# Performance work log

Hardware: AMD Instinct MI355X
Metric: run time of the kernel (lower is better)

## Reference

```python
import jax, jax.numpy as jnp
import numpy as np

B, N, T, F = 4, 5000, 16, 64
E = 80000
H, C_OUT = 4, 16           # attention heads, per-head out channels
S = H * C_OUT              # stream_dim = 64
HID = 192                  # encoder hidden_dim = 3 * S
NEG_SLOPE = 0.2
EPS_SM = 1e-16             # PyG softmax eps
EPS_LN = 1e-5


def setup_inputs() -> dict:
    key = jax.random.key(0)
    ks = jax.random.split(key, 12)
    rn = lambda k, shape, s=0.1: jax.random.normal(k, shape, jnp.float32) * s
    return {
        "x_seq": rn(ks[0], (T, B, N, F), 1.0),
        "lin_w": rn(ks[1], (3, S, F)),          # per-stream GAT linear [out,in]
        "att_src": rn(ks[2], (3, H, C_OUT)),
        "att_dst": rn(ks[3], (3, H, C_OUT)),
        "gat_bias": jnp.zeros((3, S), jnp.float32),
        "w_ih": rn(ks[4], (3, 4 * S, S)),       # LSTMCell input weights (i,f,g,o)
        "w_hh": rn(ks[5], (3, 4 * S, S)),
        "b_ih": jnp.zeros((3, 4 * S), jnp.float32),
        "b_hh": jnp.zeros((3, 4 * S), jnp.float32),
        "ln_g": jnp.ones((3, S), jnp.float32),
        "ln_b": jnp.zeros((3, S), jnp.float32),
        "attn_w1": rn(ks[6], (HID // 2, 3 * S)),
        "attn_b1": jnp.zeros((HID // 2,), jnp.float32),
        "attn_w2": rn(ks[7], (3, HID // 2)),
        "attn_b2": jnp.zeros((3,), jnp.float32),
        "edge_index": jax.random.randint(ks[8], (2, E), 0, N, jnp.int32),
    }


def _batched_edges(edge_index):
    # replicate the graph B times with node-id offsets, then add self loops
    offs = (jnp.arange(B, dtype=edge_index.dtype) * N)[:, None]
    src = (edge_index[0][None, :] + offs).reshape(-1)
    dst = (edge_index[1][None, :] + offs).reshape(-1)
    loops = jnp.arange(B * N, dtype=edge_index.dtype)
    return jnp.concatenate([src, loops]), jnp.concatenate([dst, loops])


def _gat(x, src, dst, lin_w, a_src, a_dst, bias):
    # x: [B,N,F] -> out: [B,N,S]
    xt = (x.reshape(B * N, F) @ lin_w.T).reshape(B * N, H, C_OUT)
    xj, xi = xt[src], xt[dst]                               # [Eb,H,C]
    a = jnp.einsum('ehc,hc->eh', xj, a_src) + jnp.einsum('ehc,hc->eh', xi, a_dst)
    a = jax.nn.leaky_relu(a, NEG_SLOPE)
    amax = jax.ops.segment_max(a, dst, num_segments=B * N)  # segment-softmax over target
    ex = jnp.exp(a - amax[dst])
    den = jax.ops.segment_sum(ex, dst, num_segments=B * N)
    alpha = ex / (den[dst] + EPS_SM)
    out = jax.ops.segment_sum(xj * alpha[..., None], dst, num_segments=B * N)
    return out.reshape(B, N, S) + bias


def _cell(x, h, c, src, dst, lin_w, a_s, a_d, gb, wih, whh, bih, bhh, g, b):
    # one TemporalGNNCell step; h,c: [B*N,S]
    sp = _gat(x, src, dst, lin_w, a_s, a_d, gb).reshape(B * N, S)
    gates = sp @ wih.T + bih + h @ whh.T + bhh
    i, f, gg, o = jnp.split(gates, 4, axis=-1)
    c_new = jax.nn.sigmoid(f) * c + jax.nn.sigmoid(i) * jnp.tanh(gg)
    h_new = jax.nn.sigmoid(o) * jnp.tanh(c_new)
    mu = h_new.mean(-1, keepdims=True)
    var = ((h_new - mu) ** 2).mean(-1, keepdims=True)
    h_ln = (h_new - mu) / jnp.sqrt(var + EPS_LN) * g + b
    return h_ln, c_new


def reference(x_seq, lin_w, att_src, att_dst, gat_bias, w_ih, w_hh, b_ih, b_hh,
              ln_g, ln_b, attn_w1, attn_b1, attn_w2, attn_b2, edge_index):
    src, dst = _batched_edges(edge_index)
    z = jnp.zeros((B * N, S), x_seq.dtype)
    hf = cf = hm = cm = hs = cs = z
    outs = []
    for t in range(T):
        x_t = x_seq[t]
        hf, cf = _cell(x_t, hf, cf, src, dst, lin_w[0], att_src[0], att_dst[0], gat_bias[0],
                       w_ih[0], w_hh[0], b_ih[0], b_hh[0], ln_g[0], ln_b[0])
        if t % 15 == 0:
            hm, cm = _cell(x_t, hm, cm, src, dst, lin_w[1], att_src[1], att_dst[1], gat_bias[1],
                           w_ih[1], w_hh[1], b_ih[1], b_hh[1], ln_g[1], ln_b[1])
        if t % 150 == 0:
            hs, cs = _cell(x_t, hs, cs, src, dst, lin_w[2], att_src[2], att_dst[2], gat_bias[2],
                           w_ih[2], w_hh[2], b_ih[2], b_hh[2], ln_g[2], ln_b[2])
        fast, med, slow = hf, hm, hs
        ms = jnp.concatenate([fast, med, slow], axis=-1)       # [B*N, 3S]
        w = jax.nn.softmax(jax.nn.relu(ms @ attn_w1.T + attn_b1) @ attn_w2.T + attn_b2, axis=-1)
        outs.append(w[:, 0:1] * fast + w[:, 1:2] * med + w[:, 2:3] * slow)
    # stack(dim=1) then permute(0,2,1,3): [B, N, T, S]
    out = jnp.stack(outs, 0).reshape(T, B, N, S).transpose(1, 2, 0, 3)
    return out
```

## Files before the change

kernel.cpp:

```cpp
#include <hip/hip_runtime.h>
#include <cstddef>

#define TT 16
#define EE 80000
#define NB 768
#define HALF_N 2500
#define NCHUNK 157
#define NTILE 313
#define XT_PAR 320512
#define AS_PAR 20032
#define WBLK 258048
#define O_LINH 0
#define O_LINL 12288
#define O_WIHH 24576
#define O_WIHL 73728
#define O_WHHH 122880
#define O_WHHL 172032
#define O_W1H  221184
#define O_W1L  239616
#define XCCREG 6164

typedef __attribute__((ext_vector_type(8))) short bf16x8;
typedef __attribute__((ext_vector_type(4))) float f32x4;

__device__ __forceinline__ float sigf(float x) { return 1.0f / (1.0f + __expf(-x)); }
__device__ __forceinline__ float lreluf(float x) { return x > 0.0f ? x : 0.2f * x; }

__device__ __forceinline__ unsigned short f2bf(float x) {
  union { float f; unsigned u; } v; v.f = x;
  unsigned r = v.u + 0x7FFF + ((v.u >> 16) & 1);
  return (unsigned short)(r >> 16);
}
__device__ __forceinline__ float bf2f(unsigned short u) {
  union { unsigned u; float f; } v; v.u = ((unsigned)u) << 16; return v.f;
}
__device__ __forceinline__ unsigned short f2h(float x) {
  _Float16 h = (_Float16)x;
  return __builtin_bit_cast(unsigned short, h);
}
__device__ __forceinline__ float h2f(unsigned short u) {
  return (float)__builtin_bit_cast(_Float16, u);
}
__device__ __forceinline__ f32x4 mfma16(bf16x8 a, bf16x8 b, f32x4 c) {
  return __builtin_amdgcn_mfma_f32_16x16x32_bf16(a, b, c, 0, 0, 0);
}
__device__ __forceinline__ void split8(const float* s, bf16x8& th, bf16x8& tl) {
#pragma unroll
  for (int i = 0; i < 8; ++i) {
    float v = s[i];
    unsigned short h = f2bf(v);
    th[i] = (short)h;
    tl[i] = (short)f2bf(v - bf2f(h));
  }
}
__device__ __forceinline__ unsigned long long ldq(const void* p) {
  return __hip_atomic_load((unsigned long long*)p, __ATOMIC_RELAXED, __HIP_MEMORY_SCOPE_AGENT);
}
__device__ __forceinline__ float ldf(const float* p) {
  return __hip_atomic_load((float*)p, __ATOMIC_RELAXED, __HIP_MEMORY_SCOPE_AGENT);
}
__device__ __forceinline__ int ldi(const int* p) {
  return __hip_atomic_load((int*)p, __ATOMIC_RELAXED, __HIP_MEMORY_SCOPE_AGENT);
}
__device__ __forceinline__ float4 ldv4(const float* p) {
  union { unsigned long long q[2]; float4 v; } u;
  u.q[0] = ldq(p); u.q[1] = ldq(p + 2); return u.v;
}

struct P {
  const float *x_seq, *att_src, *att_dst, *gat_bias, *ln_g, *ln_b, *b1, *w2, *b2;
  const float *lin_w, *w_ih, *w_hh, *b_ih, *b_hh, *w1;
  const int* eidx;
  float* out;
  unsigned short* xt;
  float *as, *ad;
  float *cmg, *csg;
  unsigned short* wblk;
  float* bsum;
  int *deg, *cnt, *startp, *adj;
  int *reg, *gcnt, *ggen, *g0;
};

__device__ __forceinline__ void mbar(int* cnt, int* gen, int size, int& rnd) {
  __syncthreads();
  ++rnd;
  if (threadIdx.x == 0) {
    int v = __hip_atomic_fetch_add(cnt, 1, __ATOMIC_RELAXED, __HIP_MEMORY_SCOPE_AGENT) + 1;
    if (v == size * rnd) {
      __hip_atomic_store(gen, rnd, __ATOMIC_RELAXED, __HIP_MEMORY_SCOPE_AGENT);
    } else {
      while (__hip_atomic_load(gen, __ATOMIC_RELAXED, __HIP_MEMORY_SCOPE_AGENT) < rnd)
        __builtin_amdgcn_s_sleep(4);
    }
  }
  __builtin_amdgcn_fence(__ATOMIC_ACQUIRE, "workgroup");
  __syncthreads();
}

__device__ void phaseA(const float* xbase, const unsigned short* linH, const unsigned short* linL,
                       const float* attS, const float* attD,
                       unsigned short* xtC, float* asC, float* adC, int rb, int lane) {
  const int l15 = lane & 15, lg = lane >> 4;
  int gm = rb * 16 + l15; if (gm > 4999) gm = 4999;
  const float* arow = xbase + (size_t)gm * 64;
  bf16x8 aH[2], aL[2];
#pragma unroll
  for (int ch = 0; ch < 2; ++ch) {
    float4 u0 = *reinterpret_cast<const float4*>(arow + ch * 32 + lg * 8);
    float4 u1 = *reinterpret_cast<const float4*>(arow + ch * 32 + lg * 8 + 4);
    float v[8] = {u0.x, u0.y, u0.z, u0.w, u1.x, u1.y, u1.z, u1.w};
    bf16x8 th, tl;
#pragma unroll
    for (int i = 0; i < 8; ++i) {
      unsigned short hi = f2bf(v[i]);
      th[i] = (short)hi;
      tl[i] = (short)f2bf(v[i] - bf2f(hi));
    }
    aH[ch] = th; aL[ch] = tl;
  }
  f32x4 acc[4];
#pragma unroll
  for (int nf = 0; nf < 4; ++nf) acc[nf] = (f32x4){0.f, 0.f, 0.f, 0.f};
#pragma unroll
  for (int nf = 0; nf < 4; ++nf) {
#pragma unroll
    for (int ch = 0; ch < 2; ++ch) {
      size_t wo = (size_t)(nf * 16 + l15) * 64 + ch * 32 + lg * 8;
      bf16x8 bH = *reinterpret_cast<const bf16x8*>(linH + wo);
      bf16x8 bL = *reinterpret_cast<const bf16x8*>(linL + wo);
      acc[nf] = mfma16(aH[ch], bH, acc[nf]);
      acc[nf] = mfma16(aH[ch], bL, acc[nf]);
      acc[nf] = mfma16(aL[ch], bH, acc[nf]);
    }
  }
#pragma unroll
  for (int nf = 0; nf < 4; ++nf) {
    float sv = attS[nf * 16 + l15], dv = attD[nf * 16 + l15];
#pragma unroll
    for (int r = 0; r < 4; ++r) {
      int row = rb * 16 + lg * 4 + r;
      float v = acc[nf][r];
      float ps = v * sv, pd = v * dv;
#pragma unroll
      for (int off = 1; off < 16; off <<= 1) { ps += __shfl_xor(ps, off); pd += __shfl_xor(pd, off); }
      xtC[(size_t)row * 64 + nf * 16 + l15] = f2h(v);
      if (l15 == 0) { asC[row * 4 + nf] = ps; adC[row * 4 + nf] = pd; }
    }
  }
}

__device__ void gather_node(const int* startp, const int* adj,
                            const float* asr, const float* adt, const unsigned short* xtC,
                            const float* gbias, int nh, int half, int lane,
                            float* sprow, float* alds, int* slds) {
  int s0 = startp[nh];
  int dg = startp[nh + 1] - s0;
  int nloc = half * 2500 + nh;
  float4 adv = ldv4(adt + (size_t)nloc * 4);

  float ex0 = 0.f, ex1 = 0.f, ex2 = 0.f, ex3 = 0.f;
  int src0 = 0;
  if (lane < dg) {
    src0 = adj[s0 + lane];
    float4 av = ldv4(asr + (size_t)src0 * 4);
    ex0 = __expf(lreluf(av.x + adv.x));
    ex1 = __expf(lreluf(av.y + adv.y));
    ex2 = __expf(lreluf(av.z + adv.z));
    ex3 = __expf(lreluf(av.w + adv.w));
  }
  float dn0 = ex0, dn1 = ex1, dn2 = ex2, dn3 = ex3;
  for (int e = 64 + lane; e < dg; e += 64) {
    int src = adj[s0 + e];
    float4 av = ldv4(asr + (size_t)src * 4);
    dn0 += __expf(lreluf(av.x + adv.x));
    dn1 += __expf(lreluf(av.y + adv.y));
    dn2 += __expf(lreluf(av.z + adv.z));
    dn3 += __expf(lreluf(av.w + adv.w));
  }
#pragma unroll
  for (int off = 1; off < 64; off <<= 1) {
    dn0 += __shfl_xor(dn0, off);
    dn1 += __shfl_xor(dn1, off);
    dn2 += __shfl_xor(dn2, off);
    dn3 += __shfl_xor(dn3, off);
  }
  float rd0 = 1.0f / (dn0 + 1e-16f), rd1 = 1.0f / (dn1 + 1e-16f);
  float rd2 = 1.0f / (dn2 + 1e-16f), rd3 = 1.0f / (dn3 + 1e-16f);
  if (lane < dg) {
    *reinterpret_cast<float4*>(alds + lane * 4) =
        make_float4(ex0 * rd0, ex1 * rd1, ex2 * rd2, ex3 * rd3);
    slds[lane] = src0;
  }
  const int g = lane >> 4, c = lane & 15, head = c >> 2;
  float a0 = 0.f, a1 = 0.f, a2 = 0.f, a3 = 0.f;
  int dglim = dg < 64 ? dg : 64;
  for (int e = g; e < dglim; e += 4) {
    float alpha = alds[e * 4 + head];
    int src = slds[e];
    unsigned long long q = ldq(xtC + (size_t)src * 64 + c * 4);
    a0 = fmaf(alpha, h2f((unsigned short)(q)), a0);
    a1 = fmaf(alpha, h2f((unsigned short)(q >> 16)), a1);
    a2 = fmaf(alpha, h2f((unsigned short)(q >> 32)), a2);
    a3 = fmaf(alpha, h2f((unsigned short)(q >> 48)), a3);
  }
  if (dg > 64) {
    float rdh = head == 0 ? rd0 : head == 1 ? rd1 : head == 2 ? rd2 : rd3;
    float adh = head == 0 ? adv.x : head == 1 ? adv.y : head == 2 ? adv.z : adv.w;
    for (int e = 64 + g; e < dg; e += 4) {
      int src = adj[s0 + e];
      float av = ldf(asr + (size_t)src * 4 + head);
      float alpha = __expf(lreluf(av + adh)) * rdh;
      unsigned long long q = ldq(xtC + (size_t)src * 64 + c * 4);
      a0 = fmaf(alpha, h2f((unsigned short)(q)), a0);
      a1 = fmaf(alpha, h2f((unsigned short)(q >> 16)), a1);
      a2 = fmaf(alpha, h2f((unsigned short)(q >> 32)), a2);
      a3 = fmaf(alpha, h2f((unsigned short)(q >> 48)), a3);
    }
  }
  a0 += __shfl_xor(a0, 16); a0 += __shfl_xor(a0, 32);
  a1 += __shfl_xor(a1, 16); a1 += __shfl_xor(a1, 32);
  a2 += __shfl_xor(a2, 16); a2 += __shfl_xor(a2, 32);
  a3 += __shfl_xor(a3, 16); a3 += __shfl_xor(a3, 32);
  if (g == 0) {
    float4 bz = *reinterpret_cast<const float4*>(gbias + c * 4);
    *reinterpret_cast<float4*>(sprow + c * 4) =
        make_float4(a0 + bz.x, a1 + bz.y, a2 + bz.z, a3 + bz.w);
  }
}

__device__ void mixcore(const unsigned short* w1H, const unsigned short* w1L,
                        const float* b1, const float* w2, const float* b2, float* out,
                        size_t grow0, int validrows, int t, int lane,
                        const float* hf, const float* hm, const float* hs) {
  const int l15 = lane & 15, lg = lane >> 4;
  bf16x8 aH[3][2], aL[3][2];
#pragma unroll
  for (int ch = 0; ch < 2; ++ch) {
    split8(hf + l15 * 68 + ch * 32 + lg * 8, aH[0][ch], aL[0][ch]);
    split8(hm + l15 * 68 + ch * 32 + lg * 8, aH[1][ch], aL[1][ch]);
    split8(hs + l15 * 68 + ch * 32 + lg * 8, aH[2][ch], aL[2][ch]);
  }
  f32x4 acc[6];
#pragma unroll
  for (int nf = 0; nf < 6; ++nf) acc[nf] = (f32x4){0.f, 0.f, 0.f, 0.f};
#pragma unroll
  for (int nf = 0; nf < 6; ++nf) {
#pragma unroll
    for (int s = 0; s < 3; ++s) {
#pragma unroll
      for (int ch = 0; ch < 2; ++ch) {
        size_t wo = (size_t)(nf * 16 + l15) * 192 + s * 64 + ch * 32 + lg * 8;
        bf16x8 bH = *reinterpret_cast<const bf16x8*>(w1H + wo);
        bf16x8 bL = *reinterpret_cast<const bf16x8*>(w1L + wo);
        acc[nf] = mfma16(aH[s][ch], bH, acc[nf]);
        acc[nf] = mfma16(aH[s][ch], bL, acc[nf]);
        acc[nf] = mfma16(aL[s][ch], bH, acc[nf]);
      }
    }
  }
#pragma unroll
  for (int r = 0; r < 4; ++r) {
    float p0 = 0.f, p1 = 0.f, p2 = 0.f;
#pragma unroll
    for (int nf = 0; nf < 6; ++nf) {
      int n = nf * 16 + l15;
      float hdv = fmaxf(acc[nf][r] + b1[n], 0.f);
      p0 = fmaf(hdv, w2[n], p0);
      p1 = fmaf(hdv, w2[96 + n], p1);
      p2 = fmaf(hdv, w2[192 + n], p2);
    }
#pragma unroll
    for (int off = 1; off < 16; off <<= 1) {
      p0 += __shfl_xor(p0, off); p1 += __shfl_xor(p1, off); p2 += __shfl_xor(p2, off);
    }
    float q0 = p0 + b2[0], q1 = p1 + b2[1], q2 = p2 + b2[2];
    float mx = fmaxf(q0, fmaxf(q1, q2));
    float e0 = __expf(q0 - mx), e1 = __expf(q1 - mx), e2 = __expf(q2 - mx);
    float rs = 1.0f / (e0 + e1 + e2);
    float w0 = e0 * rs, w1v = e1 * rs, w2v = e2 * rs;
    int r16 = lg * 4 + r;
    if (r16 < validrows) {
      size_t ob = ((grow0 + r16) * TT + t) * 64;
#pragma unroll
      for (int q = 0; q < 4; ++q) {
        int col = l15 + 16 * q;
        float vf = hf[r16 * 68 + col];
        float vm = hm[r16 * 68 + col];
        float vs = hs[r16 * 68 + col];
        out[ob + col] = w0 * vf + w1v * vm + w2v * vs;
      }
    }
  }
}

__device__ void phaseC(const unsigned short* WihH, const unsigned short* WihL,
                       const unsigned short* WhhH, const unsigned short* WhhL,
                       const float* bsum, const float* lng, const float* lnb,
                       float* cglob, float creg[4][4],
                       size_t grow0, int validrows, int lane,
                       const float* sp, float* h) {
  const int l15 = lane & 15, lg = lane >> 4;
  bf16x8 sH[2], sL[2], hHa[2], hLa[2];
#pragma unroll
  for (int ch = 0; ch < 2; ++ch) {
    split8(sp + l15 * 68 + ch * 32 + lg * 8, sH[ch], sL[ch]);
    split8(h + l15 * 68 + ch * 32 + lg * 8, hHa[ch], hLa[ch]);
  }
  f32x4 acc[16];
#pragma unroll
  for (int nf = 0; nf < 16; ++nf) acc[nf] = (f32x4){0.f, 0.f, 0.f, 0.f};
#pragma unroll
  for (int nf = 0; nf < 16; ++nf) {
#pragma unroll
    for (int ch = 0; ch < 2; ++ch) {
      size_t wo = (size_t)(nf * 16 + l15) * 64 + ch * 32 + lg * 8;
      bf16x8 bH = *reinterpret_cast<const bf16x8*>(WihH + wo);
      bf16x8 bL = *reinterpret_cast<const bf16x8*>(WihL + wo);
      acc[nf] = mfma16(sH[ch], bH, acc[nf]);
      acc[nf] = mfma16(sH[ch], bL, acc[nf]);
      acc[nf] = mfma16(sL[ch], bH, acc[nf]);
      bf16x8 cH = *reinterpret_cast<const bf16x8*>(WhhH + wo);
      bf16x8 cL = *reinterpret_cast<const bf16x8*>(WhhL + wo);
      acc[nf] = mfma16(hHa[ch], cH, acc[nf]);
      acc[nf] = mfma16(hHa[ch], cL, acc[nf]);
      acc[nf] = mfma16(hLa[ch], cH, acc[nf]);
    }
  }
  float hn[4][4];
#pragma unroll
  for (int cq = 0; cq < 4; ++cq) {
    int col = cq * 16 + l15;
    float bi = bsum[col], bff = bsum[64 + col], bg = bsum[128 + col], bo = bsum[192 + col];
#pragma unroll
    for (int r = 0; r < 4; ++r) {
      int r16 = lg * 4 + r;
      float gi = acc[cq][r] + bi;
      float gf = acc[cq + 4][r] + bff;
      float gg = acc[cq + 8][r] + bg;
      float go = acc[cq + 12][r] + bo;
      float cold;
      if (cglob) {
        int crow = r16 < validrows ? r16 : validrows - 1;
        cold = ldf(cglob + (grow0 + crow) * 64 + col);
      } else cold = creg[cq][r];
      float cv = sigf(gf) * cold + sigf(gi) * tanhf(gg);
      if (cglob) { if (r16 < validrows) cglob[(grow0 + r16) * 64 + col] = cv; }
      else creg[cq][r] = cv;
      hn[cq][r] = sigf(go) * tanhf(cv);
    }
  }
#pragma unroll
  for (int r = 0; r < 4; ++r) {
    float s = hn[0][r] + hn[1][r] + hn[2][r] + hn[3][r];
#pragma unroll
    for (int off = 1; off < 16; off <<= 1) s += __shfl_xor(s, off);
    float mu = s * (1.0f / 64.0f);
    float vv = 0.f;
#pragma unroll
    for (int cq = 0; cq < 4; ++cq) { float d = hn[cq][r] - mu; vv += d * d; }
#pragma unroll
    for (int off = 1; off < 16; off <<= 1) vv += __shfl_xor(vv, off);
    float rstd = rsqrtf(vv * (1.0f / 64.0f) + 1e-5f);
#pragma unroll
    for (int cq = 0; cq < 4; ++cq) {
      int col = cq * 16 + l15;
      h[(lg * 4 + r) * 68 + col] = (hn[cq][r] - mu) * rstd * lng[col] + lnb[col];
    }
  }
}

__global__ __launch_bounds__(256, 3) void mega(P p) {
  const int tid = threadIdx.x, lane = tid & 63, wv = tid >> 6, pair = wv >> 1;
  __shared__ float s8[8][16][68];
  __shared__ float al[4][256];
  __shared__ int sr[4][64];
  __shared__ int shr[2];

  const int xcd = (int)(__builtin_amdgcn_s_getreg(XCCREG) & 7);
  if (tid == 0)
    shr[0] = (int)__hip_atomic_fetch_add(&p.reg[xcd], 1, __ATOMIC_RELAXED, __HIP_MEMORY_SCOPE_AGENT);

  int grnd = 0;
  mbar(p.g0, p.g0 + 16, NB, grnd);
  if (tid == 0) shr[1] = ldi(&p.reg[xcd]);
  __syncthreads();
  const int rank = shr[0], size = shr[1];
  const int batch = xcd >> 1, half = xcd & 1;
  const size_t nodeg = (size_t)batch * 5000 + (size_t)half * 2500;

  unsigned short* xtX = p.xt + (size_t)xcd * 6 * XT_PAR;
  float* asX = p.as + (size_t)xcd * 6 * AS_PAR;
  float* adX = p.ad + (size_t)xcd * 6 * AS_PAR;
  unsigned short* w = p.wblk + (size_t)xcd * WBLK;
  float* bsum = p.bsum + xcd * 768;
  int* deg = p.deg + xcd * 2504;
  int* cnt = p.cnt + xcd * 2504;
  int* startp = p.startp + xcd * 2504;
  int* adj = p.adj + (size_t)xcd * 82504;
  int* xc = p.gcnt + xcd * 16;
  int* xg = p.ggen + xcd * 16;
  int xrnd = 0;

  for (int i = tid; i < 8 * 16 * 68; i += 256) ((float*)s8)[i] = 0.f;
  float creg[4][4];
#pragma unroll
  for (int a = 0; a < 4; ++a)
#pragma unroll
    for (int r = 0; r < 4; ++r) creg[a][r] = 0.f;

  const int st = rank * 256 + tid, stride = size * 256;

  for (int i = st; i < 160000; i += stride) {
    p.cmg[nodeg * 64 + i] = 0.f;
    p.csg[nodeg * 64 + i] = 0.f;
  }
  for (int i = st; i < 2504; i += stride) { deg[i] = 0; cnt[i] = 0; }
  for (int i = st; i < 49152; i += stride) {
    if (i < 12288) { float v = p.lin_w[i]; unsigned short h = f2bf(v); w[O_LINH + i] = h; w[O_LINL + i] = f2bf(v - bf2f(h)); }
    { float v = p.w_ih[i]; unsigned short h = f2bf(v); w[O_WIHH + i] = h; w[O_WIHL + i] = f2bf(v - bf2f(h)); }
    { float v = p.w_hh[i]; unsigned short h = f2bf(v); w[O_WHHH + i] = h; w[O_WHHL + i] = f2bf(v - bf2f(h)); }
    if (i < 18432) { float v = p.w1[i]; unsigned short h = f2bf(v); w[O_W1H + i] = h; w[O_W1L + i] = f2bf(v - bf2f(h)); }
    if (i < 768) bsum[i] = p.b_ih[i] + p.b_hh[i];
  }
  mbar(xc, xg, size, xrnd);

  for (int i = st; i < EE + 2500; i += stride) {
    if (i < EE) {
      int dst = p.eidx[EE + i];
      if ((dst >= 2500) == (half == 1)) atomicAdd(deg + (dst - half * 2500), 1);
    } else atomicAdd(deg + (i - EE), 1);
  }
  mbar(xc, xg, size, xrnd);

  if (rank == 0) {
    int* ib = (int*)&al[0][0];
    int s = 0;
    for (int j = 0; j < 10; ++j) {
      int n = tid * 10 + j;
      if (n < 2500) s += ldi(deg + n);
    }
    ib[tid] = s;
    __syncthreads();
    for (int off = 1; off < 256; off <<= 1) {
      int tv = (tid >= off) ? ib[tid - off] : 0;
      __syncthreads();
      ib[tid] += tv;
      __syncthreads();
    }
    int excl = ib[tid] - s;
    for (int j = 0; j < 10; ++j) {
      int n = tid * 10 + j;
      if (n < 2500) { startp[n] = excl; excl += ldi(deg + n); }
    }
    if (tid == 255) startp[2500] = ib[255];
    __syncthreads();
  }
  mbar(xc, xg, size, xrnd);

  for (int i = st; i < EE + 2500; i += stride) {
    if (i < EE) {
      int dst = p.eidx[EE + i];
      if ((dst >= 2500) == (half == 1)) {
        int ln = dst - half * 2500;
        int pos = atomicAdd(cnt + ln, 1);
        adj[startp[ln] + pos] = p.eidx[i];
      }
    } else {
      int n = i - EE;
      int pos = atomicAdd(cnt + n, 1);
      adj[startp[n] + pos] = half * 2500 + n;
    }
  }
  {
    const float* xb = p.x_seq + (size_t)batch * 5000 * 64;
    for (int a = rank * 4 + wv; a < 3 * NTILE; a += size * 4) {
      int cell = a / NTILE, rb = a - cell * NTILE;
      phaseA(xb, w + O_LINH + cell * 4096, w + O_LINL + cell * 4096,
             p.att_src + cell * 64, p.att_dst + cell * 64,
             xtX + (size_t)(cell * 2) * XT_PAR, asX + (size_t)(cell * 2) * AS_PAR,
             adX + (size_t)(cell * 2) * AS_PAR, rb, lane);
    }
  }
  mbar(xc, xg, size, xrnd);

  const int chunk = rank * 2 + pair;
  const bool has = chunk < NCHUNK;
  const int validrows = has ? ((2500 - chunk * 16) < 16 ? (2500 - chunk * 16) : 16) : 0;
  const size_t grow0 = nodeg + (size_t)chunk * 16;
  float* sp = &s8[pair * 4 + 0][0][0];
  float* hf = &s8[pair * 4 + 1][0][0];
  float* hm = &s8[pair * 4 + 2][0][0];
  float* hs = &s8[pair * 4 + 3][0][0];

  auto do_gather = [&](int cell, int tstep) {
    if (!has) return;
    int par = tstep & 1;
    const float* asr = asX + (size_t)(cell * 2 + par) * AS_PAR;
    const float* adt = adX + (size_t)(cell * 2 + par) * AS_PAR;
    const unsigned short* xtC = xtX + (size_t)(cell * 2 + par) * XT_PAR;
    const float* gb = p.gat_bias + cell * 64;
    int w01 = wv & 1;
    for (int j = 0; j < 8; ++j) {
      int ridx = w01 * 8 + j;
      int nh = chunk * 16 + ridx;
      float* sprow = sp + ridx * 68;
      if (nh < 2500)
        gather_node(startp, adj, asr, adt, xtC, gb, nh, half, lane, sprow, &al[wv][0], &sr[wv][0]);
      else if ((lane >> 4) == 0)
        *reinterpret_cast<float4*>(sprow + (lane & 15) * 4) = make_float4(0.f, 0.f, 0.f, 0.f);
    }
  };
  auto do_C = [&](int cell, bool domix) {
    if (!has || (wv & 1)) return;
    float* hcur = cell == 0 ? hf : (cell == 1 ? hm : hs);
    float* cg = cell == 0 ? nullptr : (cell == 1 ? p.cmg : p.csg);
    phaseC(w + O_WIHH + cell * 16384, w + O_WIHL + cell * 16384,
           w + O_WHHH + cell * 16384, w + O_WHHL + cell * 16384,
           bsum + cell * 256, p.ln_g + cell * 64, p.ln_b + cell * 64,
           cg, creg, grow0, validrows, lane, sp, hcur);
    if (domix)
      mixcore(w + O_W1H, w + O_W1L, p.b1, p.w2, p.b2, p.out, grow0, validrows,
              0, lane, hf, hm, hs);
  };

  const float* xb = p.x_seq + (size_t)batch * 5000 * 64;

  for (int t = 0; t < TT; ++t) {
    if (t != 0 && t != 15) {
      do_gather(0, t);
      __syncthreads();
      if (wv & 1) {
        int nA = (t + 1 == 15) ? 2 * NTILE : NTILE;
        const float* xbt = xb + (size_t)(t + 1) * 20000 * 64;
        for (int a = rank * 2 + pair; a < nA; a += 2 * size) {
          int cell = a >= NTILE, rb = a - cell * NTILE;
          int par = (t + 1) & 1;
          phaseA(xbt, w + O_LINH + cell * 4096, w + O_LINL + cell * 4096,
                 p.att_src + cell * 64, p.att_dst + cell * 64,
                 xtX + (size_t)(cell * 2 + par) * XT_PAR, asX + (size_t)(cell * 2 + par) * AS_PAR,
                 adX + (size_t)(cell * 2 + par) * AS_PAR, rb, lane);
        }
      } else if (has) {
        phaseC(w + O_WIHH, w + O_WIHL, w + O_WHHH, w + O_WHHL,
               bsum, p.ln_g, p.ln_b, nullptr, creg, grow0, validrows, lane, sp, hf);
        mixcore(w + O_W1H, w + O_W1L, p.b1, p.w2, p.b2, p.out, grow0, validrows, t, lane, hf, hm, hs);
      }
    } else if (t == 0) {
      do_gather(0, 0);
      __syncthreads();
      if (has && !(wv & 1))
        phaseC(w + O_WIHH, w + O_WIHL, w + O_WHHH, w + O_WHHL,
               bsum, p.ln_g, p.ln_b, nullptr, creg, grow0, validrows, lane, sp, hf);
      __syncthreads();
      do_gather(1, 0);
      __syncthreads();
      if (has && !(wv & 1))
        phaseC(w + O_WIHH + 16384, w + O_WIHL + 16384, w + O_WHHH + 16384, w + O_WHHL + 16384,
               bsum + 256, p.ln_g + 64, p.ln_b + 64, p.cmg, creg, grow0, validrows, lane, sp, hm);
      __syncthreads();
      do_gather(2, 0);
      __syncthreads();
      if (has && !(wv & 1)) {
        phaseC(w + O_WIHH + 32768, w + O_WIHL + 32768, w + O_WHHH + 32768, w + O_WHHL + 32768,
               bsum + 512, p.ln_g + 128, p.ln_b + 128, p.csg, creg, grow0, validrows, lane, sp, hs);
        mixcore(w + O_W1H, w + O_W1L, p.b1, p.w2, p.b2, p.out, grow0, validrows, 0, lane, hf, hm, hs);
      }
      __syncthreads();
      const float* xbt = xb + (size_t)20000 * 64;
      for (int a = rank * 4 + wv; a < NTILE; a += size * 4)
        phaseA(xbt, w + O_LINH, w + O_LINL, p.att_src, p.att_dst,
               xtX + XT_PAR, asX + AS_PAR, adX + AS_PAR, a, lane);
    } else {
      do_gather(0, 15);
      __syncthreads();
      if (has && !(wv & 1))
        phaseC(w + O_WIHH, w + O_WIHL, w + O_WHHH, w + O_WHHL,
               bsum, p.ln_g, p.ln_b, nullptr, creg, grow0, validrows, lane, sp, hf);
      __syncthreads();
      do_gather(1, 15);
      __syncthreads();
      if (has && !(wv & 1)) {
        phaseC(w + O_WIHH + 16384, w + O_WIHL + 16384, w + O_WHHH + 16384, w + O_WHHL + 16384,
               bsum + 256, p.ln_g + 64, p.ln_b + 64, p.cmg, creg, grow0, validrows, lane, sp, hm);
        mixcore(w + O_W1H, w + O_W1L, p.b1, p.w2, p.b2, p.out, grow0, validrows, 15, lane, hf, hm, hs);
      }
    }
    mbar(xc, xg, size, xrnd);
  }
  (void)do_C;
}

extern "C" void kernel_launch(void* const* d_in, const int* in_sizes, int n_in,
                              void* d_out, int out_size, void* d_ws, size_t ws_size,
                              hipStream_t stream) {
  P p;
  p.x_seq    = (const float*)d_in[0];
  p.lin_w    = (const float*)d_in[1];
  p.att_src  = (const float*)d_in[2];
  p.att_dst  = (const float*)d_in[3];
  p.gat_bias = (const float*)d_in[4];
  p.w_ih     = (const float*)d_in[5];
  p.w_hh     = (const float*)d_in[6];
  p.b_ih     = (const float*)d_in[7];
  p.b_hh     = (const float*)d_in[8];
  p.ln_g     = (const float*)d_in[9];
  p.ln_b     = (const float*)d_in[10];
  p.w1       = (const float*)d_in[11];
  p.b1       = (const float*)d_in[12];
  p.w2       = (const float*)d_in[13];
  p.b2       = (const float*)d_in[14];
  p.eidx     = (const int*)d_in[15];
  p.out      = (float*)d_out;

  char* base = (char*)d_ws;
  size_t off = 0;
  auto alloc = [&](size_t bytes) { char* r = base + off; off += (bytes + 255) & ~(size_t)255; return r; };
  p.xt     = (unsigned short*)alloc((size_t)8 * 6 * XT_PAR * 2);
  p.as     = (float*)alloc((size_t)8 * 6 * AS_PAR * 4);
  p.ad     = (float*)alloc((size_t)8 * 6 * AS_PAR * 4);
  p.cmg    = (float*)alloc((size_t)1280000 * 4);
  p.csg    = (float*)alloc((size_t)1280000 * 4);
  p.wblk   = (unsigned short*)alloc((size_t)8 * WBLK * 2);
  p.bsum   = (float*)alloc(8 * 768 * 4);
  p.deg    = (int*)alloc(8 * 2504 * 4);
  p.cnt    = (int*)alloc(8 * 2504 * 4);
  p.startp = (int*)alloc(8 * 2504 * 4);
  p.adj    = (int*)alloc((size_t)8 * 82504 * 4);
  int* barzone = (int*)alloc(8192);
  p.reg  = barzone;
  p.gcnt = barzone + 64;
  p.ggen = barzone + 64 + 128;
  p.g0   = barzone + 64 + 256;

  hipMemsetAsync(barzone, 0, 8192, stream);
  mega<<<NB, 256, 0, stream>>>(p);
}
```

Before: 2.367 ms.

## Keep medium/slow LSTM cell state in registers and use plain vector loads

Replaces the global-memory cell-state arrays for the medium and slow streams with per-thread register arrays, since each thread always owns the same rows. The slow state is only used at t=0, so it becomes a local zeroed array. Feature buffers shrink from six to four slots: fast stays double-buffered, medium and slow get one slot each. Agent-scope atomic loads in the gather are replaced by ordinary vectorized loads, which removes their overhead but relies on the grid barrier for cross-block visibility of data that may be cached.

```diff
diff --git a/kernel.cpp b/kernel.cpp
--- a/kernel.cpp
+++ b/kernel.cpp
@@ -4,7 +4,6 @@
 #define TT 16
 #define EE 80000
 #define NB 768
-#define HALF_N 2500
 #define NCHUNK 157
 #define NTILE 313
 #define XT_PAR 320512
@@ -53,18 +52,8 @@
     tl[i] = (short)f2bf(v - bf2f(h));
   }
 }
-__device__ __forceinline__ unsigned long long ldq(const void* p) {
-  return __hip_atomic_load((unsigned long long*)p, __ATOMIC_RELAXED, __HIP_MEMORY_SCOPE_AGENT);
-}
-__device__ __forceinline__ float ldf(const float* p) {
-  return __hip_atomic_load((float*)p, __ATOMIC_RELAXED, __HIP_MEMORY_SCOPE_AGENT);
-}
 __device__ __forceinline__ int ldi(const int* p) {
   return __hip_atomic_load((int*)p, __ATOMIC_RELAXED, __HIP_MEMORY_SCOPE_AGENT);
-}
-__device__ __forceinline__ float4 ldv4(const float* p) {
-  union { unsigned long long q[2]; float4 v; } u;
-  u.q[0] = ldq(p); u.q[1] = ldq(p + 2); return u.v;
 }
 
 struct P {
@@ -74,7 +63,6 @@
   float* out;
   unsigned short* xt;
   float *as, *ad;
-  float *cmg, *csg;
   unsigned short* wblk;
   float* bsum;
   int *deg, *cnt, *startp, *adj;
@@ -156,13 +144,13 @@
   int s0 = startp[nh];
   int dg = startp[nh + 1] - s0;
   int nloc = half * 2500 + nh;
-  float4 adv = ldv4(adt + (size_t)nloc * 4);
+  float4 adv = *reinterpret_cast<const float4*>(adt + (size_t)nloc * 4);
 
   float ex0 = 0.f, ex1 = 0.f, ex2 = 0.f, ex3 = 0.f;
   int src0 = 0;
   if (lane < dg) {
     src0 = adj[s0 + lane];
-    float4 av = ldv4(asr + (size_t)src0 * 4);
+    float4 av = *reinterpret_cast<const float4*>(asr + (size_t)src0 * 4);
     ex0 = __expf(lreluf(av.x + adv.x));
     ex1 = __expf(lreluf(av.y + adv.y));
     ex2 = __expf(lreluf(av.z + adv.z));
@@ -171,7 +159,7 @@
   float dn0 = ex0, dn1 = ex1, dn2 = ex2, dn3 = ex3;
   for (int e = 64 + lane; e < dg; e += 64) {
     int src = adj[s0 + e];
-    float4 av = ldv4(asr + (size_t)src * 4);
+    float4 av = *reinterpret_cast<const float4*>(asr + (size_t)src * 4);
     dn0 += __expf(lreluf(av.x + adv.x));
     dn1 += __expf(lreluf(av.y + adv.y));
     dn2 += __expf(lreluf(av.z + adv.z));
@@ -197,24 +185,24 @@
   for (int e = g; e < dglim; e += 4) {
     float alpha = alds[e * 4 + head];
     int src = slds[e];
-    unsigned long long q = ldq(xtC + (size_t)src * 64 + c * 4);
-    a0 = fmaf(alpha, h2f((unsigned short)(q)), a0);
-    a1 = fmaf(alpha, h2f((unsigned short)(q >> 16)), a1);
-    a2 = fmaf(alpha, h2f((unsigned short)(q >> 32)), a2);
-    a3 = fmaf(alpha, h2f((unsigned short)(q >> 48)), a3);
+    ushort4 xv = *reinterpret_cast<const ushort4*>(xtC + (size_t)src * 64 + c * 4);
+    a0 = fmaf(alpha, h2f(xv.x), a0);
+    a1 = fmaf(alpha, h2f(xv.y), a1);
+    a2 = fmaf(alpha, h2f(xv.z), a2);
+    a3 = fmaf(alpha, h2f(xv.w), a3);
   }
   if (dg > 64) {
     float rdh = head == 0 ? rd0 : head == 1 ? rd1 : head == 2 ? rd2 : rd3;
     float adh = head == 0 ? adv.x : head == 1 ? adv.y : head == 2 ? adv.z : adv.w;
     for (int e = 64 + g; e < dg; e += 4) {
       int src = adj[s0 + e];
-      float av = ldf(asr + (size_t)src * 4 + head);
+      float av = asr[(size_t)src * 4 + head];
       float alpha = __expf(lreluf(av + adh)) * rdh;
-      unsigned long long q = ldq(xtC + (size_t)src * 64 + c * 4);
-      a0 = fmaf(alpha, h2f((unsigned short)(q)), a0);
-      a1 = fmaf(alpha, h2f((unsigned short)(q >> 16)), a1);
-      a2 = fmaf(alpha, h2f((unsigned short)(q >> 32)), a2);
-      a3 = fmaf(alpha, h2f((unsigned short)(q >> 48)), a3);
+      ushort4 xv = *reinterpret_cast<const ushort4*>(xtC + (size_t)src * 64 + c * 4);
+      a0 = fmaf(alpha, h2f(xv.x), a0);
+      a1 = fmaf(alpha, h2f(xv.y), a1);
+      a2 = fmaf(alpha, h2f(xv.z), a2);
+      a3 = fmaf(alpha, h2f(xv.w), a3);
     }
   }
   a0 += __shfl_xor(a0, 16); a0 += __shfl_xor(a0, 32);
@@ -296,9 +284,7 @@
 __device__ void phaseC(const unsigned short* WihH, const unsigned short* WihL,
                        const unsigned short* WhhH, const unsigned short* WhhL,
                        const float* bsum, const float* lng, const float* lnb,
-                       float* cglob, float creg[4][4],
-                       size_t grow0, int validrows, int lane,
-                       const float* sp, float* h) {
+                       float creg[4][4], int lane, const float* sp, float* h) {
   const int l15 = lane & 15, lg = lane >> 4;
   bf16x8 sH[2], sL[2], hHa[2], hLa[2];
 #pragma unroll
@@ -333,19 +319,12 @@
     float bi = bsum[col], bff = bsum[64 + col], bg = bsum[128 + col], bo = bsum[192 + col];
 #pragma unroll
     for (int r = 0; r < 4; ++r) {
-      int r16 = lg * 4 + r;
       float gi = acc[cq][r] + bi;
       float gf = acc[cq + 4][r] + bff;
       float gg = acc[cq + 8][r] + bg;
       float go = acc[cq + 12][r] + bo;
-      float cold;
-      if (cglob) {
-        int crow = r16 < validrows ? r16 : validrows - 1;
-        cold = ldf(cglob + (grow0 + crow) * 64 + col);
-      } else cold = creg[cq][r];
-      float cv = sigf(gf) * cold + sigf(gi) * tanhf(gg);
-      if (cglob) { if (r16 < validrows) cglob[(grow0 + r16) * 64 + col] = cv; }
-      else creg[cq][r] = cv;
+      float cv = sigf(gf) * creg[cq][r] + sigf(gi) * tanhf(gg);
+      creg[cq][r] = cv;
       hn[cq][r] = sigf(go) * tanhf(cv);
     }
   }
@@ -388,9 +367,9 @@
   const int batch = xcd >> 1, half = xcd & 1;
   const size_t nodeg = (size_t)batch * 5000 + (size_t)half * 2500;
 
-  unsigned short* xtX = p.xt + (size_t)xcd * 6 * XT_PAR;
-  float* asX = p.as + (size_t)xcd * 6 * AS_PAR;
-  float* adX = p.ad + (size_t)xcd * 6 * AS_PAR;
+  unsigned short* xtX = p.xt + (size_t)xcd * 4 * XT_PAR;
+  float* asX = p.as + (size_t)xcd * 4 * AS_PAR;
+  float* adX = p.ad + (size_t)xcd * 4 * AS_PAR;
   unsigned short* w = p.wblk + (size_t)xcd * WBLK;
   float* bsum = p.bsum + xcd * 768;
   int* deg = p.deg + xcd * 2504;
@@ -402,18 +381,14 @@
   int xrnd = 0;
 
   for (int i = tid; i < 8 * 16 * 68; i += 256) ((float*)s8)[i] = 0.f;
-  float creg[4][4];
+  float cregF[4][4], cregM[4][4];
 #pragma unroll
   for (int a = 0; a < 4; ++a)
 #pragma unroll
-    for (int r = 0; r < 4; ++r) creg[a][r] = 0.f;
+    for (int r = 0; r < 4; ++r) { cregF[a][r] = 0.f; cregM[a][r] = 0.f; }
 
   const int st = rank * 256 + tid, stride = size * 256;
 
-  for (int i = st; i < 160000; i += stride) {
-    p.cmg[nodeg * 64 + i] = 0.f;
-    p.csg[nodeg * 64 + i] = 0.f;
-  }
   for (int i = st; i < 2504; i += stride) { deg[i] = 0; cnt[i] = 0; }
   for (int i = st; i < 49152; i += stride) {
     if (i < 12288) { float v = p.lin_w[i]; unsigned short h = f2bf(v); w[O_LINH + i] = h; w[O_LINL + i] = f2bf(v - bf2f(h)); }
@@ -475,10 +450,11 @@
     const float* xb = p.x_seq + (size_t)batch * 5000 * 64;
     for (int a = rank * 4 + wv; a < 3 * NTILE; a += size * 4) {
       int cell = a / NTILE, rb = a - cell * NTILE;
+      int buf = (cell == 0) ? 0 : cell + 1;
       phaseA(xb, w + O_LINH + cell * 4096, w + O_LINL + cell * 4096,
              p.att_src + cell * 64, p.att_dst + cell * 64,
-             xtX + (size_t)(cell * 2) * XT_PAR, asX + (size_t)(cell * 2) * AS_PAR,
-             adX + (size_t)(cell * 2) * AS_PAR, rb, lane);
+             xtX + (size_t)buf * XT_PAR, asX + (size_t)buf * AS_PAR,
+             adX + (size_t)buf * AS_PAR, rb, lane);
     }
   }
   mbar(xc, xg, size, xrnd);
@@ -492,12 +468,11 @@
   float* hm = &s8[pair * 4 + 2][0][0];
   float* hs = &s8[pair * 4 + 3][0][0];
 
-  auto do_gather = [&](int cell, int tstep) {
+  auto do_gather = [&](int cell, int buf) {
     if (!has) return;
-    int par = tstep & 1;
-    const float* asr = asX + (size_t)(cell * 2 + par) * AS_PAR;
-    const float* adt = adX + (size_t)(cell * 2 + par) * AS_PAR;
-    const unsigned short* xtC = xtX + (size_t)(cell * 2 + par) * XT_PAR;
+    const float* asr = asX + (size_t)buf * AS_PAR;
+    const float* adt = adX + (size_t)buf * AS_PAR;
+    const unsigned short* xtC = xtX + (size_t)buf * XT_PAR;
     const float* gb = p.gat_bias + cell * 64;
     int w01 = wv & 1;
     for (int j = 0; j < 8; ++j) {
@@ -510,39 +485,27 @@
         *reinterpret_cast<float4*>(sprow + (lane & 15) * 4) = make_float4(0.f, 0.f, 0.f, 0.f);
     }
   };
-  auto do_C = [&](int cell, bool domix) {
-    if (!has || (wv & 1)) return;
-    float* hcur = cell == 0 ? hf : (cell == 1 ? hm : hs);
-    float* cg = cell == 0 ? nullptr : (cell == 1 ? p.cmg : p.csg);
-    phaseC(w + O_WIHH + cell * 16384, w + O_WIHL + cell * 16384,
-           w + O_WHHH + cell * 16384, w + O_WHHL + cell * 16384,
-           bsum + cell * 256, p.ln_g + cell * 64, p.ln_b + cell * 64,
-           cg, creg, grow0, validrows, lane, sp, hcur);
-    if (domix)
-      mixcore(w + O_W1H, w + O_W1L, p.b1, p.w2, p.b2, p.out, grow0, validrows,
-              0, lane, hf, hm, hs);
-  };
 
   const float* xb = p.x_seq + (size_t)batch * 5000 * 64;
 
   for (int t = 0; t < TT; ++t) {
     if (t != 0 && t != 15) {
-      do_gather(0, t);
+      do_gather(0, t & 1);
       __syncthreads();
       if (wv & 1) {
         int nA = (t + 1 == 15) ? 2 * NTILE : NTILE;
         const float* xbt = xb + (size_t)(t + 1) * 20000 * 64;
         for (int a = rank * 2 + pair; a < nA; a += 2 * size) {
           int cell = a >= NTILE, rb = a - cell * NTILE;
-          int par = (t + 1) & 1;
+          int buf = cell ? 2 : ((t + 1) & 1);
           phaseA(xbt, w + O_LINH + cell * 4096, w + O_LINL + cell * 4096,
                  p.att_src + cell * 64, p.att_dst + cell * 64,
-                 xtX + (size_t)(cell * 2 + par) * XT_PAR, asX + (size_t)(cell * 2 + par) * AS_PAR,
-                 adX + (size_t)(cell * 2 + par) * AS_PAR, rb, lane);
+                 xtX + (size_t)buf * XT_PAR, asX + (size_t)buf * AS_PAR,
+                 adX + (size_t)buf * AS_PAR, rb, lane);
         }
       } else if (has) {
         phaseC(w + O_WIHH, w + O_WIHL, w + O_WHHH, w + O_WHHL,
-               bsum, p.ln_g, p.ln_b, nullptr, creg, grow0, validrows, lane, sp, hf);
+               bsum, p.ln_g, p.ln_b, cregF, lane, sp, hf);
         mixcore(w + O_W1H, w + O_W1L, p.b1, p.w2, p.b2, p.out, grow0, validrows, t, lane, hf, hm, hs);
       }
     } else if (t == 0) {
@@ -550,19 +513,24 @@
       __syncthreads();
       if (has && !(wv & 1))
         phaseC(w + O_WIHH, w + O_WIHL, w + O_WHHH, w + O_WHHL,
-               bsum, p.ln_g, p.ln_b, nullptr, creg, grow0, validrows, lane, sp, hf);
-      __syncthreads();
-      do_gather(1, 0);
+               bsum, p.ln_g, p.ln_b, cregF, lane, sp, hf);
+      __syncthreads();
+      do_gather(1, 2);
       __syncthreads();
       if (has && !(wv & 1))
         phaseC(w + O_WIHH + 16384, w + O_WIHL + 16384, w + O_WHHH + 16384, w + O_WHHL + 16384,
-               bsum + 256, p.ln_g + 64, p.ln_b + 64, p.cmg, creg, grow0, validrows, lane, sp, hm);
-      __syncthreads();
-      do_gather(2, 0);
+               bsum + 256, p.ln_g + 64, p.ln_b + 64, cregM, lane, sp, hm);
+      __syncthreads();
+      do_gather(2, 3);
       __syncthreads();
       if (has && !(wv & 1)) {
+        float cregS[4][4];
+#pragma unroll
+        for (int a = 0; a < 4; ++a)
+#pragma unroll
+          for (int r = 0; r < 4; ++r) cregS[a][r] = 0.f;
         phaseC(w + O_WIHH + 32768, w + O_WIHL + 32768, w + O_WHHH + 32768, w + O_WHHL + 32768,
-               bsum + 512, p.ln_g + 128, p.ln_b + 128, p.csg, creg, grow0, validrows, lane, sp, hs);
+               bsum + 512, p.ln_g + 128, p.ln_b + 128, cregS, lane, sp, hs);
         mixcore(w + O_W1H, w + O_W1L, p.b1, p.w2, p.b2, p.out, grow0, validrows, 0, lane, hf, hm, hs);
       }
       __syncthreads();
@@ -571,23 +539,22 @@
         phaseA(xbt, w + O_LINH, w + O_LINL, p.att_src, p.att_dst,
                xtX + XT_PAR, asX + AS_PAR, adX + AS_PAR, a, lane);
     } else {
-      do_gather(0, 15);
+      do_gather(0, 1);
       __syncthreads();
       if (has && !(wv & 1))
         phaseC(w + O_WIHH, w + O_WIHL, w + O_WHHH, w + O_WHHL,
-               bsum, p.ln_g, p.ln_b, nullptr, creg, grow0, validrows, lane, sp, hf);
-      __syncthreads();
-      do_gather(1, 15);
+               bsum, p.ln_g, p.ln_b, cregF, lane, sp, hf);
+      __syncthreads();
+      do_gather(1, 2);
       __syncthreads();
       if (has && !(wv & 1)) {
         phaseC(w + O_WIHH + 16384, w + O_WIHL + 16384, w + O_WHHH + 16384, w + O_WHHL + 16384,
-               bsum + 256, p.ln_g + 64, p.ln_b + 64, p.cmg, creg, grow0, validrows, lane, sp, hm);
+               bsum + 256, p.ln_g + 64, p.ln_b + 64, cregM, lane, sp, hm);
         mixcore(w + O_W1H, w + O_W1L, p.b1, p.w2, p.b2, p.out, grow0, validrows, 15, lane, hf, hm, hs);
       }
     }
     mbar(xc, xg, size, xrnd);
   }
-  (void)do_C;
 }
 
 extern "C" void kernel_launch(void* const* d_in, const int* in_sizes, int n_in,
@@ -615,11 +582,9 @@
   char* base = (char*)d_ws;
   size_t off = 0;
   auto alloc = [&](size_t bytes) { char* r = base + off; off += (bytes + 255) & ~(size_t)255; return r; };
-  p.xt     = (unsigned short*)alloc((size_t)8 * 6 * XT_PAR * 2);
-  p.as     = (float*)alloc((size_t)8 * 6 * AS_PAR * 4);
-  p.ad     = (float*)alloc((size_t)8 * 6 * AS_PAR * 4);
-  p.cmg    = (float*)alloc((size_t)1280000 * 4);
-  p.csg    = (float*)alloc((size_t)1280000 * 4);
+  p.xt     = (unsigned short*)alloc((size_t)8 * 4 * XT_PAR * 2);
+  p.as     = (float*)alloc((size_t)8 * 4 * AS_PAR * 4);
+  p.ad     = (float*)alloc((size_t)8 * 4 * AS_PAR * 4);
   p.wblk   = (unsigned short*)alloc((size_t)8 * WBLK * 2);
   p.bsum   = (float*)alloc(8 * 768 * 4);
   p.deg    = (int*)alloc(8 * 2504 * 4);
```

After: 2.653 ms. 1.12x slower.
